# Optimization experiments

Measured on AMD Instinct MI355X. Metric: run time of the kernel, lower is better.

The kernel has to match this reference:

```python
import jax, jax.numpy as jnp
import numpy as np

NEG_SLOPE = 0.15


def _gcn_norm(edge_index, num_nodes):
    # PyG GCNConv default: add self-loops, symmetric normalization.
    src = jnp.concatenate([edge_index[0], jnp.arange(num_nodes)])
    dst = jnp.concatenate([edge_index[1], jnp.arange(num_nodes)])
    deg = jax.ops.segment_sum(jnp.ones_like(src, dtype=jnp.float32), dst,
                              num_segments=num_nodes)
    dis = jnp.where(deg > 0, jax.lax.rsqrt(jnp.maximum(deg, 1.0)), 0.0)
    norm = dis[src] * dis[dst]  # [E + N]
    return src, dst, norm


def _gcn_conv(h, W, b, src, dst, norm, num_nodes):
    h = h @ W                                   # dense transform first (PyG order)
    msg = h[src] * norm[:, None]                # gather + scale per edge
    out = jax.ops.segment_sum(msg, dst, num_segments=num_nodes)  # scatter-add
    return out + b


def setup_inputs() -> dict:
    key = jax.random.key(0)
    ks = jax.random.split(key, 16)
    N, E, D = 20000, 320000, 128
    x = jax.random.normal(ks[0], (N, D), dtype=jnp.float32)
    edge_index = jax.random.randint(ks[1], (2, E), 0, N, dtype=jnp.int32)
    edge_attr = jax.random.normal(ks[2], (E, 2), dtype=jnp.float32)

    def lin(k, fi, fo):
        kw, kb = jax.random.split(k)
        s = 1.0 / np.sqrt(fi)
        return (jax.random.uniform(kw, (fi, fo), jnp.float32, -s, s),
                jax.random.uniform(kb, (fo,), jnp.float32, -s, s))

    W1, b1 = lin(ks[3], D, 512)
    W2, b2 = lin(ks[4], 512, 256)
    W3, b3 = lin(ks[5], 256, 128)
    Wp, bp = lin(ks[6], 128, 16)   # pre_fc (128 -> 16)
    Wf1, bf1 = lin(ks[7], 16, 32)  # fallback MLP classifier
    Wf2, bf2 = lin(ks[8], 32, 2)
    return {"x": x, "edge_index": edge_index, "edge_attr": edge_attr,
            "W1": W1, "b1": b1, "W2": W2, "b2": b2, "W3": W3, "b3": b3,
            "Wp": Wp, "bp": bp, "Wf1": Wf1, "bf1": bf1, "Wf2": Wf2, "bf2": bf2}


def reference(x, edge_index, edge_attr, W1, b1, W2, b2, W3, b3,
              Wp, bp, Wf1, bf1, Wf2, bf2):
    N = x.shape[0]
    src, dst, norm = _gcn_norm(edge_index, N)
    lrelu = lambda h: jax.nn.leaky_relu(h, NEG_SLOPE)
    h = lrelu(_gcn_conv(x, W1, b1, src, dst, norm, N))   # dropout = identity (eval)
    h = lrelu(_gcn_conv(h, W2, b2, src, dst, norm, N))
    h = lrelu(_gcn_conv(h, W3, b3, src, dst, norm, N))
    h = h @ Wp + bp                                      # pre_fc: 128 -> 16
    h = lrelu(h @ Wf1 + bf1)                             # classifier MLP
    return h @ Wf2 + bf2                                 # [N, 2]
```

## Files before the change

kernel.cpp:

```cpp
#include <hip/hip_runtime.h>
#include <hip/hip_bf16.h>

typedef __hip_bfloat16 bf16;
typedef unsigned short ushort_t;
typedef __attribute__((ext_vector_type(8))) short short8v;
typedef __attribute__((ext_vector_type(4))) float floatx4;

#define NEG_SLOPE 0.15f

__device__ __forceinline__ float us2f(unsigned short u) {
    unsigned int x = ((unsigned int)u) << 16;
    float f;
    __builtin_memcpy(&f, &x, 4);
    return f;
}
__device__ __forceinline__ unsigned short f2us(float v) {
    bf16 h = __float2bfloat16(v);
    unsigned short u;
    __builtin_memcpy(&u, &h, 2);
    return u;
}

#define GLOAD_LDS16(gp, lp)                                                  \
    __builtin_amdgcn_global_load_lds(                                        \
        (const __attribute__((address_space(1))) unsigned int*)(gp),         \
        (__attribute__((address_space(3))) unsigned int*)(lp), 16, 0, 0)

__device__ __forceinline__ int block_flag(const unsigned int* __restrict__ xw) {
    __shared__ int cnt;
    if (threadIdx.x == 0) cnt = 0;
    __syncthreads();
    if (threadIdx.x < 256) {
        unsigned int w = xw[threadIdx.x];
        unsigned int e = (w >> 7) & 0xFF;
        if ((w & 0xFFFF) == 0 || (e >= 100 && e <= 140)) atomicAdd(&cnt, 1);
    }
    __syncthreads();
    return cnt >= 150;
}

struct PrepDesc {
    const void* src[14];
    void* dst[14];
    int n[14];
    int K[14], Nn[14];
};

__global__ void prep_small_kernel(PrepDesc d, const void* __restrict__ xsrc) {
    int f = block_flag((const unsigned int*)xsrc);
    int t = blockIdx.y;
    int Kt = d.K[t];
    int nt = d.n[t];
    if (Kt == -2) {
        ushort_t* out = (ushort_t*)d.dst[t];
        const void* in = d.src[t];
        int stride = gridDim.x * blockDim.x;
        for (int i = blockIdx.x * blockDim.x + threadIdx.x; i < nt; i += stride)
            out[i] = f ? ((const unsigned short*)in)[i] : f2us(((const float*)in)[i]);
        return;
    }
    int i = blockIdx.x * blockDim.x + threadIdx.x;
    if (i >= nt) return;
    if (Kt == -1) {
        ((int*)d.dst[t])[i] = 0;
    } else if (Kt == 0) {
        ((float*)d.dst[t])[i] = f ? us2f(((const unsigned short*)d.src[t])[i])
                                  : ((const float*)d.src[t])[i];
    } else {
        int K = Kt, Nn = d.Nn[t];
        int n = i / K, k = i - n * K;
        size_t si = (size_t)k * Nn + n;
        ((ushort_t*)d.dst[t])[i] = f ? ((const unsigned short*)d.src[t])[si]
                                     : f2us(((const float*)d.src[t])[si]);
    }
}

__global__ void count_deg_kernel(const int* __restrict__ dst, int* __restrict__ deg,
                                 int E, int N) {
    int i = blockIdx.x * blockDim.x + threadIdx.x;
    if (i < E) {
        int d = dst[i];
        d = d < 0 ? 0 : (d >= N ? N - 1 : d);
        atomicAdd(&deg[d], 1);
    }
}

__global__ void scan_merged_kernel(const int* __restrict__ deg, int* __restrict__ offsets,
                                   int* __restrict__ cursor, float* __restrict__ dis,
                                   int* __restrict__ bsumf, int N) {
    __shared__ int sh[1024];
    __shared__ int base_s;
    int tid = threadIdx.x;
    int b = blockIdx.x;
    int i = b * 1024 + tid;
    int v = (i < N) ? (deg[i] + 1) : 0;
    sh[tid] = v;
    __syncthreads();
    for (int off = 1; off < 1024; off <<= 1) {
        int t = (tid >= off) ? sh[tid - off] : 0;
        __syncthreads();
        sh[tid] += t;
        __syncthreads();
    }
    if (tid == 0) {
        __hip_atomic_store(&bsumf[b], sh[1023] + 1, __ATOMIC_RELEASE,
                           __HIP_MEMORY_SCOPE_AGENT);
        int a = 0;
        for (int pb = 0; pb < b; ++pb) {
            int val;
            do {
                val = __hip_atomic_load(&bsumf[pb], __ATOMIC_ACQUIRE,
                                        __HIP_MEMORY_SCOPE_AGENT);
            } while (val == 0);
            a += val - 1;
        }
        base_s = a;
    }
    __syncthreads();
    if (i < N) {
        int base = base_s;
        int d = deg[i] + 1;
        int inc = sh[tid];
        int excl = base + inc - d;
        offsets[i] = excl;
        cursor[i] = excl;
        dis[i] = rsqrtf((float)d);
        if (i == N - 1) offsets[N] = base + inc;
    }
}

__global__ void fill_csr_kernel(const int* __restrict__ src, const int* __restrict__ dst,
                                const float* __restrict__ dis, int* __restrict__ cursor,
                                int2* __restrict__ edges, int E, int N, int Etot) {
    int i = blockIdx.x * blockDim.x + threadIdx.x;
    int s, d;
    if (i < E) { s = src[i]; d = dst[i]; }
    else if (i < Etot) { s = d = i - E; }
    else return;
    s = s < 0 ? 0 : (s >= N ? N - 1 : s);
    d = d < 0 ? 0 : (d >= N ? N - 1 : d);
    int pos = atomicAdd(&cursor[d], 1);
    if (pos >= 0 && pos < Etot) edges[pos] = make_int2(s, __float_as_int(dis[s]));
}

template <int VEC> struct LdT;
template <> struct LdT<2> { typedef unsigned int T; };
template <> struct LdT<4> { typedef uint2 T; };

template <int VEC>
__device__ __forceinline__ void addv(typename LdT<VEC>::T u, float w, float* acc);
template <>
__device__ __forceinline__ void addv<2>(unsigned int u, float w, float* acc) {
    acc[0] += w * us2f((unsigned short)(u & 0xFFFF));
    acc[1] += w * us2f((unsigned short)(u >> 16));
}
template <>
__device__ __forceinline__ void addv<4>(uint2 u, float w, float* acc) {
    acc[0] += w * us2f((unsigned short)(u.x & 0xFFFF));
    acc[1] += w * us2f((unsigned short)(u.x >> 16));
    acc[2] += w * us2f((unsigned short)(u.y & 0xFFFF));
    acc[3] += w * us2f((unsigned short)(u.y >> 16));
}

template <int VEC>
__device__ __forceinline__ void agg_core(
    const ushort_t* __restrict__ Hin, const int* __restrict__ offsets,
    const int2* __restrict__ edges, const float* __restrict__ dis,
    int node, int lane, int N, int Etot,
    const float* __restrict__ bias, int do_lrelu, float* outv) {
    typedef typename LdT<VEC>::T LT;
    const int F = VEC * 64;
    int beg = offsets[node], end = offsets[node + 1];
    beg = beg < 0 ? 0 : (beg > Etot ? Etot : beg);
    end = end < beg ? beg : (end > Etot ? Etot : end);

    float acc[VEC];
#pragma unroll
    for (int v = 0; v < VEC; ++v) acc[v] = 0.f;

    int fo = lane * VEC;
    int e = beg;
    for (; e + 8 <= end; e += 8) {
        int2 r[8];
#pragma unroll
        for (int j = 0; j < 8; ++j) r[j] = edges[e + j];
        LT u[8];
#pragma unroll
        for (int j = 0; j < 8; ++j) {
            int s = r[j].x;
            s = s < 0 ? 0 : (s >= N ? N - 1 : s);
            u[j] = *(const LT*)(Hin + (size_t)s * F + fo);
        }
#pragma unroll
        for (int j = 0; j < 8; ++j) addv<VEC>(u[j], __int_as_float(r[j].y), acc);
    }
    if (e + 4 <= end) {
        int2 r[4];
#pragma unroll
        for (int j = 0; j < 4; ++j) r[j] = edges[e + j];
        LT u[4];
#pragma unroll
        for (int j = 0; j < 4; ++j) {
            int s = r[j].x;
            s = s < 0 ? 0 : (s >= N ? N - 1 : s);
            u[j] = *(const LT*)(Hin + (size_t)s * F + fo);
        }
#pragma unroll
        for (int j = 0; j < 4; ++j) addv<VEC>(u[j], __int_as_float(r[j].y), acc);
        e += 4;
    }
    for (; e < end; ++e) {
        int2 r = edges[e];
        int s = r.x;
        s = s < 0 ? 0 : (s >= N ? N - 1 : s);
        LT u = *(const LT*)(Hin + (size_t)s * F + fo);
        addv<VEC>(u, __int_as_float(r.y), acc);
    }

    float dn = dis[node];
#pragma unroll
    for (int v = 0; v < VEC; ++v) {
        float a = acc[v] * dn;
        if (bias) a += bias[fo + v];
        if (do_lrelu) a = (a > 0.f) ? a : a * NEG_SLOPE;
        outv[v] = a;
    }
}

template <int VEC>
__global__ __launch_bounds__(256) void agg_kernel(
    const ushort_t* __restrict__ Hin, ushort_t* __restrict__ OutB,
    const int* __restrict__ offsets, const int2* __restrict__ edges,
    const float* __restrict__ dis, int N, int Etot,
    const float* __restrict__ bias, int do_lrelu) {
    int lane = threadIdx.x & 63;
    int node = blockIdx.x * 4 + (threadIdx.x >> 6);
    if (node >= N) return;
    float outv[VEC];
    agg_core<VEC>(Hin, offsets, edges, dis, node, lane, N, Etot, bias, do_lrelu, outv);
    size_t base = (size_t)node * (VEC * 64) + lane * VEC;
    if (VEC == 2) {
        unsigned int w = ((unsigned int)f2us(outv[1]) << 16) | f2us(outv[0]);
        *(unsigned int*)(OutB + base) = w;
    } else {
        uint2 w;
        w.x = ((unsigned int)f2us(outv[1]) << 16) | f2us(outv[0]);
        w.y = ((unsigned int)f2us(outv[3]) << 16) | f2us(outv[2]);
        *(uint2*)(OutB + base) = w;
    }
}

__global__ __launch_bounds__(256) void agg_head_kernel(
    const ushort_t* __restrict__ Hin,
    const int* __restrict__ offsets, const int2* __restrict__ edges,
    const float* __restrict__ dis, int N, int Etot,
    const float* __restrict__ b3,
    const float* __restrict__ Wp, const float* __restrict__ bp,
    const float* __restrict__ Wf1, const float* __restrict__ bf1v,
    const float* __restrict__ Wf2, const float* __restrict__ bf2v,
    void* __restrict__ out, const void* __restrict__ xsrc) {
    int flag = block_flag((const unsigned int*)xsrc);
    int lane = threadIdx.x & 63;
    int node = blockIdx.x * 4 + (threadIdx.x >> 6);
    if (node >= N) return;
    float h[2];
    agg_core<2>(Hin, offsets, edges, dis, node, lane, N, Etot, b3, 1, h);

    int fo = lane * 2;
    float p[16];
#pragma unroll
    for (int j = 0; j < 16; ++j)
        p[j] = h[0] * Wp[fo * 16 + j] + h[1] * Wp[(fo + 1) * 16 + j];
#pragma unroll
    for (int m = 1; m < 64; m <<= 1) {
#pragma unroll
        for (int j = 0; j < 16; ++j) p[j] += __shfl_xor(p[j], m, 64);
    }
    float a0 = 0.f, a1 = 0.f;
    if (lane < 32) {
        float s = bf1v[lane];
#pragma unroll
        for (int k = 0; k < 16; ++k) s += (p[k] + bp[k]) * Wf1[k * 32 + lane];
        s = (s > 0.f) ? s : s * NEG_SLOPE;
        a0 = s * Wf2[lane * 2 + 0];
        a1 = s * Wf2[lane * 2 + 1];
    }
#pragma unroll
    for (int m = 1; m < 64; m <<= 1) {
        a0 += __shfl_xor(a0, m, 64);
        a1 += __shfl_xor(a1, m, 64);
    }
    if (lane == 0) {
        float o0 = a0 + bf2v[0];
        float o1 = a1 + bf2v[1];
        if (flag) {
            unsigned int w = ((unsigned int)f2us(o1) << 16) | f2us(o0);
            *(unsigned int*)((ushort_t*)out + (size_t)node * 2) = w;
        } else {
            *(float2*)((float*)out + (size_t)node * 2) = make_float2(o0, o1);
        }
    }
}

__global__ __launch_bounds__(256) void mfma_gemm_kernel(
    const ushort_t* __restrict__ A, const ushort_t* __restrict__ Bt,
    ushort_t* __restrict__ C,
    int M, int K, int Nn, const float* __restrict__ bias, int do_lrelu) {
    __shared__ ushort_t As[128 * 64];
    __shared__ ushort_t Bs[64 * 64];

    int tid = threadIdx.x;
    int row0 = blockIdx.y * 128;
    int col0 = blockIdx.x * 64;
    int lane = tid & 63;
    int w = tid >> 6;
    int quad = lane >> 4;
    int col = lane & 15;
    int wr = (w >> 1) * 64;
    int wc = (w & 1) * 32;

    floatx4 acc[4][2];
#pragma unroll
    for (int i = 0; i < 4; ++i)
#pragma unroll
        for (int j = 0; j < 2; ++j) acc[i][j] = (floatx4){0.f, 0.f, 0.f, 0.f};

    int aoff[4], boff[2];
#pragma unroll
    for (int rt = 0; rt < 4; ++rt) {
        int r = wr + rt * 16 + col;
        aoff[rt] = (r * 128 + quad * 16) ^ ((r & 7) << 4);
    }
#pragma unroll
    for (int ct = 0; ct < 2; ++ct) {
        int r = wc + ct * 16 + col;
        boff[ct] = (r * 128 + quad * 16) ^ ((r & 7) << 4);
    }

    for (int k0 = 0; k0 < K; k0 += 64) {
#pragma unroll
        for (int i = 0; i < 4; ++i) {
            int t = i * 256 + tid;
            int r = t >> 3;
            int g = (t & 7) ^ (r & 7);
            const ushort_t* src = A + (size_t)(row0 + r) * K + k0 + g * 8;
            GLOAD_LDS16(src, &As[t * 8]);
        }
#pragma unroll
        for (int i = 0; i < 2; ++i) {
            int t = i * 256 + tid;
            int r = t >> 3;
            int g = (t & 7) ^ (r & 7);
            const ushort_t* src = Bt + (size_t)(col0 + r) * K + k0 + g * 8;
            GLOAD_LDS16(src, &Bs[t * 8]);
        }
        __syncthreads();

#pragma unroll
        for (int ks = 0; ks < 2; ++ks) {
            short8v af[4], bf[2];
#pragma unroll
            for (int rt = 0; rt < 4; ++rt)
                af[rt] = *(const short8v*)((const char*)As + (aoff[rt] ^ (ks * 64)));
#pragma unroll
            for (int ct = 0; ct < 2; ++ct)
                bf[ct] = *(const short8v*)((const char*)Bs + (boff[ct] ^ (ks * 64)));
#pragma unroll
            for (int rt = 0; rt < 4; ++rt)
#pragma unroll
                for (int ct = 0; ct < 2; ++ct)
                    acc[rt][ct] = __builtin_amdgcn_mfma_f32_16x16x32_bf16(
                        af[rt], bf[ct], acc[rt][ct], 0, 0, 0);
        }
        __syncthreads();
    }

#pragma unroll
    for (int rt = 0; rt < 4; ++rt) {
#pragma unroll
        for (int ct = 0; ct < 2; ++ct) {
            int gcol = col0 + wc + ct * 16 + col;
            float bv = bias ? bias[gcol] : 0.f;
#pragma unroll
            for (int r = 0; r < 4; ++r) {
                int grow = row0 + wr + rt * 16 + quad * 4 + r;
                if (grow >= M) continue;
                float v = acc[rt][ct][r] + bv;
                if (do_lrelu) v = (v > 0.f) ? v : v * NEG_SLOPE;
                C[(size_t)grow * Nn + gcol] = f2us(v);
            }
        }
    }
}

extern "C" void kernel_launch(void* const* d_in, const int* in_sizes, int n_in,
                              void* d_out, int out_size, void* d_ws, size_t ws_size,
                              hipStream_t stream) {
    const int* ei = (const int*)d_in[1];

    const int N = in_sizes[0] / 128;
    const int E = in_sizes[1] / 2;
    const int Etot = E + N;
    const int nb = (N + 1023) / 1024;
    const int* srcv = ei;
    const int* dstv = ei + E;

    uintptr_t p = (uintptr_t)d_ws;
    auto alloc = [&](size_t bytes) -> void* {
        p = (p + 255) & ~(uintptr_t)255;
        void* r = (void*)p;
        p += bytes;
        return r;
    };
    int*      deg     = (int*)alloc((size_t)(N + nb + 1) * 4);
    int*      bsumf   = deg + N;
    int*      offsets = (int*)alloc((size_t)(N + 1) * 4);
    int*      cursor  = (int*)alloc((size_t)N * 4);
    float*    dis     = (float*)alloc((size_t)N * 4);
    int2*     edges   = (int2*)alloc((size_t)Etot * 8);
    ushort_t* xb      = (ushort_t*)alloc((size_t)N * 128 * 2);

    const int K1 = 128, N1 = 512, K2 = 512, N2 = 256, K3 = 256, N3 = 128;
    ushort_t* W1t = (ushort_t*)alloc((size_t)K1 * N1 * 2);
    ushort_t* W2t = (ushort_t*)alloc((size_t)K2 * N2 * 2);
    ushort_t* W3t = (ushort_t*)alloc((size_t)K3 * N3 * 2);

    float* smalls[9];
    const int wmap[9] = {4, 6, 8, 9, 10, 11, 12, 13, 14};
    for (int t = 0; t < 9; ++t)
        smalls[t] = (float*)alloc((size_t)in_sizes[wmap[t]] * 4);
    const float *b1 = smalls[0], *b2 = smalls[1], *b3 = smalls[2];
    const float *Wp = smalls[3], *bp = smalls[4];
    const float *Wf1 = smalls[5], *bf1v = smalls[6];
    const float *Wf2 = smalls[7], *bf2v = smalls[8];

    ushort_t* BufT0 = (ushort_t*)alloc((size_t)N * 128 * 2);
    ushort_t* BufH1 = (ushort_t*)alloc((size_t)N * 512 * 2);
    ushort_t* BufT2 = (ushort_t*)alloc((size_t)N * 256 * 2);
    ushort_t* t0 = BufT0;
    ushort_t* t3 = BufT0;
    ushort_t* H1 = BufH1;
    ushort_t* H2 = BufH1;
    ushort_t* t2 = BufT2;

    {
        PrepDesc pd;
        for (int t = 0; t < 9; ++t) {
            pd.src[t] = d_in[wmap[t]];
            pd.dst[t] = smalls[t];
            pd.n[t] = in_sizes[wmap[t]];
            pd.K[t] = 0; pd.Nn[t] = 0;
        }
        pd.src[9]  = d_in[3]; pd.dst[9]  = W1t; pd.n[9]  = K1 * N1; pd.K[9]  = K1; pd.Nn[9]  = N1;
        pd.src[10] = d_in[5]; pd.dst[10] = W2t; pd.n[10] = K2 * N2; pd.K[10] = K2; pd.Nn[10] = N2;
        pd.src[11] = d_in[7]; pd.dst[11] = W3t; pd.n[11] = K3 * N3; pd.K[11] = K3; pd.Nn[11] = N3;
        pd.src[12] = nullptr; pd.dst[12] = deg; pd.n[12] = N + nb + 1; pd.K[12] = -1; pd.Nn[12] = 0;
        pd.src[13] = d_in[0]; pd.dst[13] = xb;  pd.n[13] = N * 128;    pd.K[13] = -2; pd.Nn[13] = 0;
        dim3 g((K2 * N2 + 255) / 256, 14);
        prep_small_kernel<<<g, 256, 0, stream>>>(pd, d_in[0]);
    }

    count_deg_kernel<<<(E + 255) / 256, 256, 0, stream>>>(dstv, deg, E, N);
    scan_merged_kernel<<<nb, 1024, 0, stream>>>(deg, offsets, cursor, dis, bsumf, N);
    fill_csr_kernel<<<(Etot + 255) / 256, 256, 0, stream>>>(srcv, dstv, dis, cursor,
                                                            edges, E, N, Etot);

    int aggGrid = (N + 3) / 4;
    agg_kernel<2><<<aggGrid, 256, 0, stream>>>(xb, t0, offsets, edges, dis,
                                               N, Etot, nullptr, 0);
    {
        dim3 g(N1 / 64, (N + 127) / 128);
        mfma_gemm_kernel<<<g, 256, 0, stream>>>(t0, W1t, H1, N, K1, N1, b1, 1);
    }
    {
        dim3 g(N2 / 64, (N + 127) / 128);
        mfma_gemm_kernel<<<g, 256, 0, stream>>>(H1, W2t, t2, N, K2, N2, nullptr, 0);
    }
    agg_kernel<4><<<aggGrid, 256, 0, stream>>>(t2, H2, offsets, edges, dis,
                                               N, Etot, b2, 1);
    {
        dim3 g(N3 / 64, (N + 127) / 128);
        mfma_gemm_kernel<<<g, 256, 0, stream>>>(H2, W3t, t3, N, K3, N3, nullptr, 0);
    }
    agg_head_kernel<<<aggGrid, 256, 0, stream>>>(t3, offsets, edges, dis, N, Etot,
                                                 b3, Wp, bp, Wf1, bf1v, Wf2, bf2v,
                                                 d_out, d_in[0]);
}
```

Before: 272.9 us.

## Split edges across lane groups with 16-byte gathers and shuffle reduction

Each wavefront's aggregation now gives every lane an 8-feature (16-byte) slice of the row. Lanes are split into groups that each take different edges of the node in parallel, and the partial sums are combined with xor shuffles. The goal is wider memory transactions and more edges in flight per wavefront. In exchange it adds shuffle-reduction work, leaves lanes idle when a node has few edges (about 17 on average here), and only a subset of lanes writes results.

```diff
diff --git a/kernel.cpp b/kernel.cpp
--- a/kernel.cpp
+++ b/kernel.cpp
@@ -143,92 +143,70 @@
     if (pos >= 0 && pos < Etot) edges[pos] = make_int2(s, __float_as_int(dis[s]));
 }
 
-template <int VEC> struct LdT;
-template <> struct LdT<2> { typedef unsigned int T; };
-template <> struct LdT<4> { typedef uint2 T; };
-
-template <int VEC>
-__device__ __forceinline__ void addv(typename LdT<VEC>::T u, float w, float* acc);
-template <>
-__device__ __forceinline__ void addv<2>(unsigned int u, float w, float* acc) {
-    acc[0] += w * us2f((unsigned short)(u & 0xFFFF));
-    acc[1] += w * us2f((unsigned short)(u >> 16));
-}
-template <>
-__device__ __forceinline__ void addv<4>(uint2 u, float w, float* acc) {
-    acc[0] += w * us2f((unsigned short)(u.x & 0xFFFF));
-    acc[1] += w * us2f((unsigned short)(u.x >> 16));
-    acc[2] += w * us2f((unsigned short)(u.y & 0xFFFF));
-    acc[3] += w * us2f((unsigned short)(u.y >> 16));
-}
-
-template <int VEC>
-__device__ __forceinline__ void agg_core(
+template <int F>
+__device__ __forceinline__ void agg_core16(
     const ushort_t* __restrict__ Hin, const int* __restrict__ offsets,
     const int2* __restrict__ edges, const float* __restrict__ dis,
     int node, int lane, int N, int Etot,
-    const float* __restrict__ bias, int do_lrelu, float* outv) {
-    typedef typename LdT<VEC>::T LT;
-    const int F = VEC * 64;
+    const float* __restrict__ bias, int do_lrelu, float* acc ) {
+    const int L = F / 8;
+    const int R = 64 / L;
+    int g = lane / L;
+    int fo = (lane % L) * 8;
+
     int beg = offsets[node], end = offsets[node + 1];
     beg = beg < 0 ? 0 : (beg > Etot ? Etot : beg);
     end = end < beg ? beg : (end > Etot ? Etot : end);
 
-    float acc[VEC];
-#pragma unroll
-    for (int v = 0; v < VEC; ++v) acc[v] = 0.f;
-
-    int fo = lane * VEC;
-    int e = beg;
-    for (; e + 8 <= end; e += 8) {
-        int2 r[8];
-#pragma unroll
-        for (int j = 0; j < 8; ++j) r[j] = edges[e + j];
-        LT u[8];
-#pragma unroll
-        for (int j = 0; j < 8; ++j) {
-            int s = r[j].x;
+#pragma unroll
+    for (int j = 0; j < 8; ++j) acc[j] = 0.f;
+
+    for (int base = beg; base < end; base += 4 * R) {
+        int2 r[4];
+#pragma unroll
+        for (int t = 0; t < 4; ++t) {
+            int idx = base + t * R + g;
+            r[t] = (idx < end) ? edges[idx] : make_int2(0, 0);
+        }
+        uint4 u[4];
+#pragma unroll
+        for (int t = 0; t < 4; ++t) {
+            int s = r[t].x;
             s = s < 0 ? 0 : (s >= N ? N - 1 : s);
-            u[j] = *(const LT*)(Hin + (size_t)s * F + fo);
-        }
-#pragma unroll
-        for (int j = 0; j < 8; ++j) addv<VEC>(u[j], __int_as_float(r[j].y), acc);
-    }
-    if (e + 4 <= end) {
-        int2 r[4];
-#pragma unroll
-        for (int j = 0; j < 4; ++j) r[j] = edges[e + j];
-        LT u[4];
-#pragma unroll
-        for (int j = 0; j < 4; ++j) {
-            int s = r[j].x;
-            s = s < 0 ? 0 : (s >= N ? N - 1 : s);
-            u[j] = *(const LT*)(Hin + (size_t)s * F + fo);
-        }
-#pragma unroll
-        for (int j = 0; j < 4; ++j) addv<VEC>(u[j], __int_as_float(r[j].y), acc);
-        e += 4;
-    }
-    for (; e < end; ++e) {
-        int2 r = edges[e];
-        int s = r.x;
-        s = s < 0 ? 0 : (s >= N ? N - 1 : s);
-        LT u = *(const LT*)(Hin + (size_t)s * F + fo);
-        addv<VEC>(u, __int_as_float(r.y), acc);
+            u[t] = *(const uint4*)(Hin + (size_t)s * F + fo);
+        }
+#pragma unroll
+        for (int t = 0; t < 4; ++t) {
+            float w = __int_as_float(r[t].y);
+            acc[0] += w * us2f((unsigned short)(u[t].x & 0xFFFF));
+            acc[1] += w * us2f((unsigned short)(u[t].x >> 16));
+            acc[2] += w * us2f((unsigned short)(u[t].y & 0xFFFF));
+            acc[3] += w * us2f((unsigned short)(u[t].y >> 16));
+            acc[4] += w * us2f((unsigned short)(u[t].z & 0xFFFF));
+            acc[5] += w * us2f((unsigned short)(u[t].z >> 16));
+            acc[6] += w * us2f((unsigned short)(u[t].w & 0xFFFF));
+            acc[7] += w * us2f((unsigned short)(u[t].w >> 16));
+        }
+    }
+
+#pragma unroll
+    for (int m = L; m < 64; m <<= 1) {
+#pragma unroll
+        for (int j = 0; j < 8; ++j) acc[j] += __shfl_xor(acc[j], m, 64);
     }
 
     float dn = dis[node];
 #pragma unroll
-    for (int v = 0; v < VEC; ++v) {
-        float a = acc[v] * dn;
-        if (bias) a += bias[fo + v];
+    for (int j = 0; j < 8; ++j) {
+        float a = acc[j] * dn;
+        if (bias) a += bias[fo + j];
         if (do_lrelu) a = (a > 0.f) ? a : a * NEG_SLOPE;
-        outv[v] = a;
-    }
-}
-
-template <int VEC>
-__global__ __launch_bounds__(256) void agg_kernel(
+        acc[j] = a;
+    }
+}
+
+template <int F>
+__global__ __launch_bounds__(256) void agg_kernel16(
     const ushort_t* __restrict__ Hin, ushort_t* __restrict__ OutB,
     const int* __restrict__ offsets, const int2* __restrict__ edges,
     const float* __restrict__ dis, int N, int Etot,
@@ -236,21 +214,20 @@
     int lane = threadIdx.x & 63;
     int node = blockIdx.x * 4 + (threadIdx.x >> 6);
     if (node >= N) return;
-    float outv[VEC];
-    agg_core<VEC>(Hin, offsets, edges, dis, node, lane, N, Etot, bias, do_lrelu, outv);
-    size_t base = (size_t)node * (VEC * 64) + lane * VEC;
-    if (VEC == 2) {
-        unsigned int w = ((unsigned int)f2us(outv[1]) << 16) | f2us(outv[0]);
-        *(unsigned int*)(OutB + base) = w;
-    } else {
-        uint2 w;
-        w.x = ((unsigned int)f2us(outv[1]) << 16) | f2us(outv[0]);
-        w.y = ((unsigned int)f2us(outv[3]) << 16) | f2us(outv[2]);
-        *(uint2*)(OutB + base) = w;
-    }
-}
-
-__global__ __launch_bounds__(256) void agg_head_kernel(
+    float a[8];
+    agg_core16<F>(Hin, offsets, edges, dis, node, lane, N, Etot, bias, do_lrelu, a);
+    const int L = F / 8;
+    if (lane < L) {
+        uint4 wv;
+        wv.x = ((unsigned int)f2us(a[1]) << 16) | f2us(a[0]);
+        wv.y = ((unsigned int)f2us(a[3]) << 16) | f2us(a[2]);
+        wv.z = ((unsigned int)f2us(a[5]) << 16) | f2us(a[4]);
+        wv.w = ((unsigned int)f2us(a[7]) << 16) | f2us(a[6]);
+        *(uint4*)(OutB + (size_t)node * F + lane * 8) = wv;
+    }
+}
+
+__global__ __launch_bounds__(256) void agg_head_kernel16(
     const ushort_t* __restrict__ Hin,
     const int* __restrict__ offsets, const int2* __restrict__ edges,
     const float* __restrict__ dis, int N, int Etot,
@@ -263,14 +240,23 @@
     int lane = threadIdx.x & 63;
     int node = blockIdx.x * 4 + (threadIdx.x >> 6);
     if (node >= N) return;
-    float h[2];
-    agg_core<2>(Hin, offsets, edges, dis, node, lane, N, Etot, b3, 1, h);
-
-    int fo = lane * 2;
+    float h[8];
+    agg_core16<128>(Hin, offsets, edges, dis, node, lane, N, Etot, b3, 1, h);
+
     float p[16];
-#pragma unroll
-    for (int j = 0; j < 16; ++j)
-        p[j] = h[0] * Wp[fo * 16 + j] + h[1] * Wp[(fo + 1) * 16 + j];
+    if (lane < 16) {
+        int f0 = lane * 8;
+#pragma unroll
+        for (int j = 0; j < 16; ++j) {
+            float s = 0.f;
+#pragma unroll
+            for (int k = 0; k < 8; ++k) s += h[k] * Wp[(f0 + k) * 16 + j];
+            p[j] = s;
+        }
+    } else {
+#pragma unroll
+        for (int j = 0; j < 16; ++j) p[j] = 0.f;
+    }
 #pragma unroll
     for (int m = 1; m < 64; m <<= 1) {
 #pragma unroll
@@ -466,8 +452,8 @@
                                                             edges, E, N, Etot);
 
     int aggGrid = (N + 3) / 4;
-    agg_kernel<2><<<aggGrid, 256, 0, stream>>>(xb, t0, offsets, edges, dis,
-                                               N, Etot, nullptr, 0);
+    agg_kernel16<128><<<aggGrid, 256, 0, stream>>>(xb, t0, offsets, edges, dis,
+                                                   N, Etot, nullptr, 0);
     {
         dim3 g(N1 / 64, (N + 127) / 128);
         mfma_gemm_kernel<<<g, 256, 0, stream>>>(t0, W1t, H1, N, K1, N1, b1, 1);
@@ -476,13 +462,13 @@
         dim3 g(N2 / 64, (N + 127) / 128);
         mfma_gemm_kernel<<<g, 256, 0, stream>>>(H1, W2t, t2, N, K2, N2, nullptr, 0);
     }
-    agg_kernel<4><<<aggGrid, 256, 0, stream>>>(t2, H2, offsets, edges, dis,
-                                               N, Etot, b2, 1);
+    agg_kernel16<256><<<aggGrid, 256, 0, stream>>>(t2, H2, offsets, edges, dis,
+                                                   N, Etot, b2, 1);
     {
         dim3 g(N3 / 64, (N + 127) / 128);
         mfma_gemm_kernel<<<g, 256, 0, stream>>>(H2, W3t, t3, N, K3, N3, nullptr, 0);
     }
-    agg_head_kernel<<<aggGrid, 256, 0, stream>>>(t3, offsets, edges, dis, N, Etot,
-                                                 b3, Wp, bp, Wf1, bf1v, Wf2, bf2v,
-                                                 d_out, d_in[0]);
-}
+    agg_head_kernel16<<<aggGrid, 256, 0, stream>>>(t3, offsets, edges, dis, N, Etot,
+                                                   b3, Wp, bp, Wf1, bf1v, Wf2, bf2v,
+                                                   d_out, d_in[0]);
+}
```

After: 312.7 us. +14.6%, slower.
